# Kernel optimization log

Measured on AMD Instinct MI355X. Metric: run time of the kernel, lower is better.

## Reference

```python
import jax, jax.numpy as jnp
import numpy as np

N_HEADS = 16
NEG_INF = -1e9


def setup_inputs() -> dict:
    key = jax.random.key(0)
    ks = jax.random.split(key, 8)
    B, S, D = 2, 2048, 1024
    HD = D // N_HEADS
    x = jax.random.normal(ks[0], (B, S, D), dtype=jnp.float32)
    # RoPE frequencies (llama-style): theta = 10000^(-2i/head_dim)
    inv_freq = 1.0 / (10000.0 ** (np.arange(0, HD, 2, dtype=np.float32) / HD))  # [HD//2]
    angles = np.arange(S, dtype=np.float32)[:, None] * inv_freq[None, :]        # [S, HD//2]
    freqs_cos = jnp.asarray(np.cos(angles))
    freqs_sin = jnp.asarray(np.sin(angles))
    # additive causal mask [1,1,S,S]
    mask = jnp.where(np.tril(np.ones((S, S), dtype=bool)), 0.0, NEG_INF).astype(jnp.float32)[None, None]
    scale = 0.02
    wq = jax.random.normal(ks[1], (D, D), dtype=jnp.float32) * scale
    wk = jax.random.normal(ks[2], (D, D), dtype=jnp.float32) * scale
    wv = jax.random.normal(ks[3], (D, D), dtype=jnp.float32) * scale
    wo = jax.random.normal(ks[4], (D, D), dtype=jnp.float32) * scale
    return {"x": x, "freqs_cos": freqs_cos, "freqs_sin": freqs_sin, "mask": mask,
            "wq": wq, "wk": wk, "wv": wv, "wo": wo}


def _rope(t, cos, sin):
    # t: [B,S,H,HD]; cos/sin: [S,HD//2]; complex mult (t0 + i t1) * (cos + i sin)
    b, s, h, hd = t.shape
    tr = t.reshape(b, s, h, hd // 2, 2)
    t0, t1 = tr[..., 0], tr[..., 1]
    c = cos[None, :, None, :]
    sn = sin[None, :, None, :]
    out = jnp.stack([t0 * c - t1 * sn, t0 * sn + t1 * c], axis=-1)
    return out.reshape(b, s, h, hd)


def reference(x, freqs_cos, freqs_sin, mask, wq, wk, wv, wo):
    b, s, d = x.shape
    hd = d // N_HEADS
    # torch Linear: y = x @ W.T
    xq = (x @ wq.T).reshape(b, s, N_HEADS, hd)
    xk = (x @ wk.T).reshape(b, s, N_HEADS, hd)
    xv = (x @ wv.T).reshape(b, s, N_HEADS, hd)
    xq = _rope(xq, freqs_cos, freqs_sin)
    xk = _rope(xk, freqs_cos, freqs_sin)
    # [B,H,S,S] scores
    scores = jnp.einsum('bqhd,bkhd->bhqk', xq, xk) / jnp.sqrt(jnp.asarray(hd, x.dtype))
    scores = scores + mask
    probs = jax.nn.softmax(scores.astype(jnp.float32), axis=-1).astype(x.dtype)
    out = jnp.einsum('bhqk,bkhd->bqhd', probs, xv).reshape(b, s, d)
    return out @ wo.T
```

## Files before the change

### kernel.cpp

```cpp
#include <hip/hip_runtime.h>
#include <hip/hip_bf16.h>
#include <cstdint>

typedef __attribute__((ext_vector_type(4))) float f32x4;
typedef __attribute__((ext_vector_type(8))) short s16x8;
typedef __attribute__((ext_vector_type(4))) unsigned short u16x4;
typedef __attribute__((ext_vector_type(2))) unsigned int u32x2;
typedef unsigned short u16;
typedef unsigned int u32;
typedef unsigned long long u64;

__device__ __forceinline__ float b2f(u16 u){ u32 v = ((u32)u)<<16; return __builtin_bit_cast(float, v); }
__device__ __forceinline__ u16 f2b(float f){
  __hip_bfloat16 h = __float2bfloat16(f);
  return __builtin_bit_cast(u16, h);
}

__device__ __forceinline__ void gld16(const void* g, void* l){
  __builtin_amdgcn_global_load_lds((const __attribute__((address_space(1))) void*)g,
                                   (__attribute__((address_space(3))) void*)l, 16, 0, 0);
}

__device__ __forceinline__ f32x4 mfma16(s16x8 a, s16x8 b, f32x4 c){
  return __builtin_amdgcn_mfma_f32_16x16x32_bf16(a, b, c, 0, 0, 0);
}

#define WS_XB   0u
#define WS_WQ   (4u<<20)
#define WS_WK   (5u<<20)
#define WS_WV   (6u<<20)
#define WS_WO   (7u<<20)
#define WS_Q    (8u<<20)
#define WS_K    (12u<<20)
#define WS_VT   (16u<<20)
#define WS_AO   (20u<<20)

#define QSCALE 0.18033688f

__global__ __launch_bounds__(256) void k_convert(const float* __restrict__ x,
    const float* __restrict__ wq, const float* __restrict__ wk,
    const float* __restrict__ wv, const float* __restrict__ wo,
    u16* __restrict__ ws){
  u32 idx = blockIdx.x*256u + threadIdx.x;
  const float* src; u16* dst;
  if (idx < (1u<<20)) { src = x + (u64)idx*4u; dst = ws + WS_XB + (u64)idx*4u; }
  else {
    u32 widx = idx - (1u<<20);
    u32 wsel = widx >> 18;
    u32 off  = (widx & ((1u<<18)-1u)) * 4u;
    const float* sp = (wsel==0u)?wq:(wsel==1u)?wk:(wsel==2u)?wv:wo;
    src = sp + off; dst = ws + WS_WQ + (u64)wsel*(1u<<20) + off;
  }
  f32x4 v = *(const f32x4*)src;
  u16x4 o = { f2b(v[0]), f2b(v[1]), f2b(v[2]), f2b(v[3]) };
  *(u16x4*)dst = o;
}

__global__ __launch_bounds__(256,2) void k_gemm(u16* __restrict__ ws, float* __restrict__ out,
    const float* __restrict__ fc, const float* __restrict__ fs, int pass){
  __shared__ char sm[65536];
  const u32 tid = threadIdx.x;
  const u32 w = tid>>6, l = tid&63u, g = l>>4, li = l&15u;
  const u32 wr = w>>1, wc = w&1u;
  u32 bx = blockIdx.x;

  const u16 *Ap, *Bp; u32 arow0, brow0; int mode;
  if (pass == 0) {
    u32 seg = bx >> 8, b2 = bx & 255u;
    if (seg < 2u) {
      Ap = ws + WS_XB; Bp = ws + (seg ? WS_WK : WS_WQ);
      arow0 = (b2 >> 3) * 128u; brow0 = (b2 & 7u) * 128u; mode = (int)seg;
    } else {
      Ap = ws + WS_WV; Bp = ws + WS_XB;
      arow0 = (b2 >> 5) * 128u; brow0 = (b2 & 31u) * 128u; mode = 2;
    }
  } else {
    Ap = ws + WS_AO; Bp = ws + WS_WO;
    arow0 = (bx >> 3) * 128u; brow0 = (bx & 7u) * 128u; mode = 3;
  }

  f32x4 acc[4][4];
  #pragma unroll
  for (u32 m=0;m<4;++m)
    #pragma unroll
    for (u32 n=0;n<4;++n) acc[m][n] = 0.0f;

  auto STAGE_G = [&](u32 s, u32 t){
    const u32 k0 = t*64u;
    #pragma unroll
    for (u32 j = 0; j < 4u; ++j) {
      u32 p = w*4096u + j*1024u + l*16u;
      u32 row = p >> 7, colb = p & 127u;
      u32 cS = colb ^ ((row & 7u) << 4);
      gld16(Ap + (u64)(arow0 + row)*1024u + k0 + (cS>>1), sm + s*32768u + w*4096u + j*1024u);
      gld16(Bp + (u64)(brow0 + row)*1024u + k0 + (cS>>1), sm + s*32768u + 16384u + w*4096u + j*1024u);
    }
  };

  STAGE_G(0u, 0u);
  __syncthreads();

  u32 cur = 0u;
  for (u32 t = 0; t < 16u; ++t) {
    if (t + 1u < 16u) STAGE_G(cur^1u, t+1u);
    const u32 cb = cur*32768u;
    s16x8 af[2][4], bf[2][4];
    #pragma unroll
    for (u32 kk=0;kk<2u;++kk){
      #pragma unroll
      for (u32 m=0;m<4;++m){
        u32 row = wr*64u + m*16u + li;
        af[kk][m] = *(const s16x8*)(sm + cb + row*128u + ((kk*64u + g*16u) ^ ((row&7u)<<4)));
      }
      #pragma unroll
      for (u32 n=0;n<4;++n){
        u32 row = wc*64u + n*16u + li;
        bf[kk][n] = *(const s16x8*)(sm + cb + 16384u + row*128u + ((kk*64u + g*16u) ^ ((row&7u)<<4)));
      }
    }
    #pragma unroll
    for (u32 kk=0;kk<2u;++kk)
      #pragma unroll
      for (u32 m=0;m<4;++m)
        #pragma unroll
        for (u32 n=0;n<4;++n)
          acc[m][n] = mfma16(af[kk][m], bf[kk][n], acc[m][n]);
    __syncthreads();
    cur ^= 1u;
  }

  u16* qdst = ws + WS_Q; u16* kdst = ws + WS_K; u16* vtd = ws + WS_VT;
  if (mode <= 1) {
    #pragma unroll
    for (u32 m=0;m<4;++m)
      #pragma unroll
      for (u32 n=0;n<4;++n)
        #pragma unroll
        for (u32 q=0;q<4;++q){
          u32 row = wr*64u + m*16u + 4u*g + q;
          u32 colb = (wc*64u + n*16u + li)*2u;
          *(u16*)(sm + row*256u + (colb ^ ((row&7u)<<4))) = f2b(acc[m][n][q]);
        }
    __syncthreads();
    u32 row = tid >> 1, half = tid & 1u;
    u32 r = arow0 + row;
    u32 b = r >> 11, s = r & 2047u;
    u32 h = (brow0 >> 6) + half;
    float qs = (mode==0) ? QSCALE : 1.0f;
    u16* d = ((mode==0) ? qdst : kdst) + (u64)(((b<<4)+h)*2048u + s)*64u;
    #pragma unroll
    for (u32 u0=0; u0<8u; ++u0){
      s16x8 cv = *(const s16x8*)(sm + row*256u + ((half*128u + u0*16u) ^ ((row&7u)<<4)));
      f32x4 cvv = *(const f32x4*)(fc + s*32u + u0*4u);
      f32x4 svv = *(const f32x4*)(fs + s*32u + u0*4u);
      s16x8 o;
      #pragma unroll
      for (u32 i=0;i<4;++i){
        float t0 = b2f((u16)cv[2*i]), t1 = b2f((u16)cv[2*i+1]);
        o[2*i]   = (short)f2b((t0*cvv[i] - t1*svv[i])*qs);
        o[2*i+1] = (short)f2b((t0*svv[i] + t1*cvv[i])*qs);
      }
      *(s16x8*)(d + u0*8u) = o;
    }
  } else {
    #pragma unroll
    for (u32 m=0;m<4;++m){
      u32 r0 = arow0 + wr*64u + m*16u + 4u*g;
      #pragma unroll
      for (u32 n=0;n<4;++n){
        u32 c = brow0 + wc*64u + n*16u + li;
        #pragma unroll
        for (u32 q=0;q<4;++q){
          float v = acc[m][n][q];
          u32 r = r0 + q;
          if (mode == 2) vtd[(u64)r*4096u + c] = f2b(v);
          else           out[(u64)r*1024u + c] = v;
        }
      }
    }
  }
}

__global__ __launch_bounds__(256,4) void k_attn(u16* __restrict__ ws){
  __shared__ char sm[40960];
  const u32 tid = threadIdx.x;
  const u32 w = tid>>6, l = tid&63u, g = l>>4, li = l&15u;
  u32 bx = blockIdx.x;
  u32 qt = 31u - (bx >> 5);
  u32 bh = bx & 31u;
  u32 b = bh >> 4, h = bh & 15u;
  const u16* Q  = ws + WS_Q + (u64)bh*2048u*64u;
  const u16* Kp = ws + WS_K + (u64)bh*2048u*64u;
  const u16* Vt = ws + WS_VT + (u64)(h*64u)*4096u + b*2048u;
  u16* AO = ws + WS_AO;
  const u32 qw = qt*64u + w*16u;

  s16x8 qa[2];
  #pragma unroll
  for (u32 kk=0;kk<2;++kk)
    qa[kk] = *(const s16x8*)(Q + (u64)(qw + li)*64u + kk*32u + g*8u);

  s16x8 ones;
  #pragma unroll
  for (u32 i=0;i<8;++i) ones[i] = (short)0x3F80;

  f32x4 o[4]; f32x4 lsum;
  #pragma unroll
  for (u32 n=0;n<4;++n) o[n] = 0.0f;
  lsum = 0.0f;

  char* pl = sm + 32768 + w*2048u;
  const u32 nt = qt + 1u;

  const u32 f0 = w*2u;
  u32 kof[2], vof[2];
  #pragma unroll
  for (u32 j=0;j<2u;++j){
    u32 f = f0 + j;
    kof[j] = ((f>>1)*16u + li)*64u  + (f&1u)*32u + g*8u;
    vof[j] = ((f>>1)*16u + li)*4096u + (f&1u)*32u + g*8u;
  }
  auto STAGE = [&](u32 s, u32 kvb){
    #pragma unroll
    for (u32 j=0;j<2u;++j){
      u32 f = f0 + j;
      gld16(Kp + (u64)kvb*64u + kof[j], sm + s*16384u + f*1024u);
      gld16(Vt + (u64)vof[j] + kvb,     sm + s*16384u + 8192u + f*1024u);
    }
  };

  STAGE(0u, 0u);
  __syncthreads();

  u32 cur = 0u;
  for (u32 t = 0; t < nt; ++t) {
    const u32 kvb = t*64u;
    if (t + 1u < nt) STAGE(cur^1u, kvb + 64u);
    const char* kb = sm + cur*16384u + l*16u;

    s16x8 kf[8];
    #pragma unroll
    for (u32 f=0; f<8u; ++f)
      kf[f] = *(const s16x8*)(kb + f*1024u);

    f32x4 sv[4];
    #pragma unroll
    for (u32 n=0;n<4;++n) sv[n] = 0.0f;
    #pragma unroll
    for (u32 n=0;n<4;++n)
      #pragma unroll
      for (u32 kk=0;kk<2u;++kk)
        sv[n] = mfma16(kf[n*2u+kk], qa[kk], sv[n]);

    if (t == nt - 1u) {
      #pragma unroll
      for (u32 n=0;n<4;++n)
        #pragma unroll
        for (u32 r=0;r<4;++r)
          if (kvb + n*16u + 4u*g + r > qw + li) sv[n][r] = -1e9f;
    }
    #pragma unroll
    for (u32 n=0;n<4;++n){
      f32x4 p;
      #pragma unroll
      for (u32 r=0;r<4;++r) p[r] = exp2f(sv[n][r]);
      u32 w0, w1;
      asm("v_cvt_pk_bf16_f32 %0, %1, %2" : "=v"(w0) : "v"(p[0]), "v"(p[1]));
      asm("v_cvt_pk_bf16_f32 %0, %1, %2" : "=v"(w1) : "v"(p[2]), "v"(p[3]));
      u32x2 pw = { w0, w1 };
      *(u32x2*)(pl + li*128u + ((n*32u + g*8u) ^ ((li&7u)<<4))) = pw;
    }
    #pragma unroll
    for (u32 kk=0;kk<2u;++kk){
      s16x8 pa = *(const s16x8*)(pl + li*128u + ((kk*64u + g*16u) ^ ((li&7u)<<4)));
      lsum = mfma16(pa, ones, lsum);
      #pragma unroll
      for (u32 n=0;n<4;++n){
        s16x8 vf = *(const s16x8*)(kb + 8192u + (n*2u+kk)*1024u);
        o[n] = mfma16(pa, vf, o[n]);
      }
    }
    __syncthreads();
    cur ^= 1u;
  }

  #pragma unroll
  for (u32 r=0;r<4;++r){
    float inv = 1.0f / lsum[r];
    u32 qr = qw + 4u*g + r;
    #pragma unroll
    for (u32 n=0;n<4;++n){
      u32 hd = n*16u + li;
      AO[((u64)(b*2048u + qr))*1024u + h*64u + hd] = f2b(o[n][r] * inv);
    }
  }
}

extern "C" void kernel_launch(void* const* d_in, const int* in_sizes, int n_in,
                              void* d_out, int out_size, void* d_ws, size_t ws_size,
                              hipStream_t stream) {
  const float* x  = (const float*)d_in[0];
  const float* fc = (const float*)d_in[1];
  const float* fs = (const float*)d_in[2];
  const float* wq = (const float*)d_in[4];
  const float* wk = (const float*)d_in[5];
  const float* wv = (const float*)d_in[6];
  const float* wo = (const float*)d_in[7];
  u16* ws = (u16*)d_ws;
  float* out = (float*)d_out;

  k_convert<<<8192, 256, 0, stream>>>(x, wq, wk, wv, wo, ws);
  k_gemm  <<<768,  256, 0, stream>>>(ws, out, fc, fs, 0);
  k_attn  <<<1024, 256, 0, stream>>>(ws);
  k_gemm  <<<256,  256, 0, stream>>>(ws, out, fc, fs, 1);
}
```

Measured before the change: 111.1 us.

## Halve GEMM K-tile and store LDS in MFMA fragment order for higher occupancy

```diff
diff --git a/kernel.cpp b/kernel.cpp
--- a/kernel.cpp
+++ b/kernel.cpp
@@ -56,9 +56,9 @@
   *(u16x4*)dst = o;
 }
 
-__global__ __launch_bounds__(256,2) void k_gemm(u16* __restrict__ ws, float* __restrict__ out,
+__global__ __launch_bounds__(256,5) void k_gemm(u16* __restrict__ ws, float* __restrict__ out,
     const float* __restrict__ fc, const float* __restrict__ fs, int pass){
-  __shared__ char sm[65536];
+  __shared__ char sm[32768];
   const u32 tid = threadIdx.x;
   const u32 w = tid>>6, l = tid&63u, g = l>>4, li = l&15u;
   const u32 wr = w>>1, wc = w&1u;
@@ -85,15 +85,21 @@
     #pragma unroll
     for (u32 n=0;n<4;++n) acc[m][n] = 0.0f;
 
+  const u32 fA = w*2u;
+  u32 frow[2];
+  #pragma unroll
+  for (u32 j=0;j<2u;++j){
+    u32 f = fA + j;
+    frow[j] = (f>>2)*64u + (f&3u)*16u + li;
+  }
+  const u32 fcol = g*8u;
   auto STAGE_G = [&](u32 s, u32 t){
-    const u32 k0 = t*64u;
-    #pragma unroll
-    for (u32 j = 0; j < 4u; ++j) {
-      u32 p = w*4096u + j*1024u + l*16u;
-      u32 row = p >> 7, colb = p & 127u;
-      u32 cS = colb ^ ((row & 7u) << 4);
-      gld16(Ap + (u64)(arow0 + row)*1024u + k0 + (cS>>1), sm + s*32768u + w*4096u + j*1024u);
-      gld16(Bp + (u64)(brow0 + row)*1024u + k0 + (cS>>1), sm + s*32768u + 16384u + w*4096u + j*1024u);
+    const u32 k0 = t*32u;
+    #pragma unroll
+    for (u32 j=0;j<2u;++j){
+      u32 f = fA + j;
+      gld16(Ap + (u64)(arow0 + frow[j])*1024u + k0 + fcol, sm + s*16384u + f*1024u);
+      gld16(Bp + (u64)(brow0 + frow[j])*1024u + k0 + fcol, sm + s*16384u + 8192u + f*1024u);
     }
   };
 
@@ -101,30 +107,19 @@
   __syncthreads();
 
   u32 cur = 0u;
-  for (u32 t = 0; t < 16u; ++t) {
-    if (t + 1u < 16u) STAGE_G(cur^1u, t+1u);
-    const u32 cb = cur*32768u;
-    s16x8 af[2][4], bf[2][4];
-    #pragma unroll
-    for (u32 kk=0;kk<2u;++kk){
-      #pragma unroll
-      for (u32 m=0;m<4;++m){
-        u32 row = wr*64u + m*16u + li;
-        af[kk][m] = *(const s16x8*)(sm + cb + row*128u + ((kk*64u + g*16u) ^ ((row&7u)<<4)));
-      }
-      #pragma unroll
-      for (u32 n=0;n<4;++n){
-        u32 row = wc*64u + n*16u + li;
-        bf[kk][n] = *(const s16x8*)(sm + cb + 16384u + row*128u + ((kk*64u + g*16u) ^ ((row&7u)<<4)));
-      }
-    }
-    #pragma unroll
-    for (u32 kk=0;kk<2u;++kk)
-      #pragma unroll
-      for (u32 m=0;m<4;++m)
-        #pragma unroll
-        for (u32 n=0;n<4;++n)
-          acc[m][n] = mfma16(af[kk][m], bf[kk][n], acc[m][n]);
+  for (u32 t = 0; t < 32u; ++t) {
+    if (t + 1u < 32u) STAGE_G(cur^1u, t+1u);
+    const char* kb = sm + cur*16384u + l*16u;
+    s16x8 af[4], bf[4];
+    #pragma unroll
+    for (u32 m=0;m<4;++m) af[m] = *(const s16x8*)(kb + (wr*4u+m)*1024u);
+    #pragma unroll
+    for (u32 n=0;n<4;++n) bf[n] = *(const s16x8*)(kb + 8192u + (wc*4u+n)*1024u);
+    #pragma unroll
+    for (u32 m=0;m<4;++m)
+      #pragma unroll
+      for (u32 n=0;n<4;++n)
+        acc[m][n] = mfma16(af[m], bf[n], acc[m][n]);
     __syncthreads();
     cur ^= 1u;
   }
```

Measured after the change: 154.3 us. +39.0%, slower.
